# Kernel optimization log

Hardware: AMD Instinct MI355X
Metric: run time of the kernel (lower is better)

The kernel has to match this reference:

```python
import jax, jax.numpy as jnp
import numpy as np

# --- config constants (from working_memory config) ---
R = 3.9; STRENGTH = 0.1; N_ITER = 10                      # logistic map
I0 = 1.0; OMEGA = 1.0; KWAVE = 2.0; ALPHA_BASE = 1.0      # Padilha wave
LC = 0.5; DE = 2.0; CHIRP_N = 1; AMIN = 0.1; AMAX = 3.0
FD = 1.5; T = 0.0                                          # fractal dim, time
ATT_ALPHA = 1.5; EPS = 1e-10                               # spectral filter
FCI = 0.7; STAB = 0.8; DEMAND = 0.6                        # neurotransmitter drives
BASE = 0.5; SENS = 1.0; DECAY = 0.1

B, S, D4 = 4, 2048, 1024  # batch, seq_len (= memory_size), embed_dim*4


def hamilton(a, b):
    # quaternion (Hamilton) product; last dim split into 4 component blocks
    aw, ax, ay, az = jnp.split(a, 4, axis=-1)
    bw, bx, by, bz = jnp.split(b, 4, axis=-1)
    w = aw * bw - ax * bx - ay * by - az * bz
    x = aw * bx + ax * bw + ay * bz - az * by
    y = aw * by - ax * bz + ay * bw + az * bx
    z = aw * bz + ax * by - ay * bx + az * bw
    return jnp.concatenate([w, x, y, z], axis=-1)


def setup_inputs() -> dict:
    key = jax.random.key(0)
    ks = jax.random.split(key, 8)
    sc = 0.02
    return {
        "query": jax.random.normal(ks[0], (B, S, D4), jnp.float32),
        "memory": jax.random.normal(ks[1], (B, S, D4), jnp.float32),
        "Wq": jax.random.normal(ks[2], (D4, D4), jnp.float32) * sc,
        "bq": jnp.zeros((D4,), jnp.float32),
        "Wk": jax.random.normal(ks[3], (D4, D4), jnp.float32) * sc,
        "bk": jnp.zeros((D4,), jnp.float32),
        "Wv": jax.random.normal(ks[4], (D4, D4), jnp.float32) * sc,
        "bv": jnp.zeros((D4,), jnp.float32),
    }


def reference(query, memory, Wq, bq, Wk, bk, Wv, bv):
    # 1) chaotic modulation of query (logistic map on sigmoid(||x||))
    s = jax.nn.sigmoid(jnp.linalg.norm(query, axis=-1))  # [B,S]
    for _ in range(N_ITER):
        s = R * s * (1.0 - s)
    q = query * (1.0 + STRENGTH * (s[..., None] - 0.5))

    # 2) Padilha wave modulation along sequence
    seq = q.shape[1]
    alpha = float(np.clip(ALPHA_BASE * (1.0 + LC * (FD - DE) / DE), AMIN, AMAX))
    beta = 2 * CHIRP_N + 1 - 2 * FD
    lam = jnp.arange(seq, dtype=q.dtype) / seq
    wave = I0 * jnp.sin(OMEGA * T + alpha * lam) * jnp.cos(OMEGA * T - KWAVE * lam + beta * lam ** 2)
    q = q * (1.0 + 0.1 * wave[None, :, None])

    # 3) neurotransmitter scalar modulation of memory (one decay step from baseline)
    dop = (1 - DECAY) * BASE + DECAY * jax.nn.sigmoid(jnp.float32(FCI * SENS))
    ser = (1 - DECAY) * BASE + DECAY * jax.nn.sigmoid(jnp.float32(STAB * SENS))
    nor = (1 - DECAY) * BASE + DECAY * jax.nn.sigmoid(jnp.float32(DEMAND * SENS))
    mem = memory * (0.4 * dop + 0.3 * ser + 0.3 * nor)

    # 4) quaternionic spectral attention
    Q = q @ Wq.T + bq
    K = mem @ Wk.T + bk
    V = mem @ Wv.T + bv
    Qf = jnp.fft.fft(Q, axis=-2)
    Kf = jnp.fft.fft(K, axis=-2)
    Vf = jnp.fft.fft(V, axis=-2)
    kidx = jnp.arange(seq, dtype=jnp.float32)
    filt = jnp.exp(1j * ATT_ALPHA * jnp.arctan(jnp.log(kidx + EPS)))[None, :, None]
    QK = hamilton(Qf * filt, Kf * filt)
    QKV = hamilton(QK, Vf * filt)
    attended = jnp.fft.ifft(QKV, axis=-2).real.astype(query.dtype)
    return attended
```

## Files before the change

### kernel.cpp

```cpp
#include <hip/hip_runtime.h>
#include <hip/hip_fp16.h>
#include <math.h>

#define S 2048
#define D4 1024
#define NB 4
#define HS 1026
#define TWOPI 6.283185307179586f

typedef __attribute__((ext_vector_type(8))) short bf16x8;
typedef __attribute__((ext_vector_type(4))) float f32x4;

__device__ __forceinline__ float2 cmul(float2 a, float2 b){
  return make_float2(a.x*b.x - a.y*b.y, a.x*b.y + a.y*b.x);
}
__device__ __forceinline__ float2 cadd(float2 a, float2 b){ return make_float2(a.x+b.x, a.y+b.y); }
__device__ __forceinline__ float2 csub(float2 a, float2 b){ return make_float2(a.x-b.x, a.y-b.y); }

__device__ __forceinline__ unsigned short f2bf(float f){
  unsigned int u = __builtin_bit_cast(unsigned int, f);
  unsigned int r = (u + 0x7FFFu + ((u >> 16) & 1u)) >> 16;
  return (unsigned short)r;
}
__device__ __forceinline__ float bf2f(unsigned short u){
  unsigned int x = (unsigned int)u << 16;
  return __builtin_bit_cast(float, x);
}

__device__ __forceinline__ void gld16(const unsigned short* g, unsigned short* l){
  __builtin_amdgcn_global_load_lds((const __attribute__((address_space(1))) unsigned int*)g,
                                   (__attribute__((address_space(3))) unsigned int*)l,
                                   16, 0, 0);
}

__device__ __forceinline__ float2 twf(const float* twr, const float* twi, int m){
  int mm = m & 1023;
  float s = (m & 1024) ? -1.f : 1.f;
  int p = mm + (mm >> 5);
  return make_float2(s * twr[p], s * twi[p]);
}

__device__ __forceinline__ void dft8_fwd(const float2 a[8], float2 o[8]){
  const float RH = 0.70710678118654752f;
  float2 b0 = cadd(a[0],a[4]), b1 = cadd(a[1],a[5]), b2 = cadd(a[2],a[6]), b3 = cadd(a[3],a[7]);
  float2 c0 = csub(a[0],a[4]);
  float2 t1 = csub(a[1],a[5]);
  float2 c1 = make_float2(RH*(t1.x + t1.y), RH*(t1.y - t1.x));
  float2 t2 = csub(a[2],a[6]);
  float2 c2 = make_float2(t2.y, -t2.x);
  float2 t3 = csub(a[3],a[7]);
  float2 c3 = make_float2(RH*(t3.y - t3.x), RH*(-(t3.x + t3.y)));
  float2 e0 = cadd(b0,b2), e1 = cadd(b1,b3);
  float2 f0 = csub(b0,b2);
  float2 f1t = csub(b1,b3); float2 f1 = make_float2(f1t.y, -f1t.x);
  o[0] = cadd(e0,e1); o[4] = csub(e0,e1);
  o[2] = cadd(f0,f1); o[6] = csub(f0,f1);
  float2 g0 = cadd(c0,c2), g1 = cadd(c1,c3);
  float2 h0 = csub(c0,c2);
  float2 h1t = csub(c1,c3); float2 h1 = make_float2(h1t.y, -h1t.x);
  o[1] = cadd(g0,g1); o[5] = csub(g0,g1);
  o[3] = cadd(h0,h1); o[7] = csub(h0,h1);
}

__device__ __forceinline__ void dft4_fwd(const float2 a[4], float2 o[4]){
  float2 b0 = cadd(a[0],a[2]), b1 = cadd(a[1],a[3]);
  float2 c0 = csub(a[0],a[2]);
  float2 c1t = csub(a[1],a[3]); float2 c1 = make_float2(c1t.y, -c1t.x);
  o[0]=cadd(b0,b1); o[2]=csub(b0,b1); o[1]=cadd(c0,c1); o[3]=csub(c0,c1);
}
__device__ __forceinline__ void dft4_inv(const float2 a[4], float2 o[4]){
  float2 b0 = cadd(a[0],a[2]), b1 = cadd(a[1],a[3]);
  float2 c0 = csub(a[0],a[2]);
  float2 c1t = csub(a[1],a[3]); float2 c1 = make_float2(-c1t.y, c1t.x);
  o[0]=cadd(b0,b1); o[2]=csub(b0,b1); o[1]=cadd(c0,c1); o[3]=csub(c0,c1);
}

__global__ __launch_bounds__(256) void prep_kernel(float* __restrict__ scale,
                                                   float2* __restrict__ gfilt,
                                                   float2* __restrict__ twg,
                                                   float alpha, float beta){
  int i = blockIdx.x * 256 + threadIdx.x;
  float lam = (float)i / (float)S;
  float w = sinf(alpha * lam) * cosf(-2.0f * lam + beta * lam * lam);
  scale[i] = 0.95f * (1.0f + 0.1f * w);
  if (i <= 1024){
    int im = (2048 - i) & 2047;
    float th1 = 1.5f * atanf(logf((float)i  + 1e-10f));
    float th2 = 1.5f * atanf(logf((float)im + 1e-10f));
    float s1, c1, s2, c2;
    sincosf(3.0f * th1, &s1, &c1);
    sincosf(3.0f * th2, &s2, &c2);
    gfilt[i] = make_float2((c1 + c2) * 0.5f, (s1 - s2) * 0.5f);
  }
  if (i < 1024){
    float s2, c2; sincosf((float)i * (TWOPI / 2048.f), &s2, &c2);
    twg[i]        = make_float2(c2, -s2);
    twg[1024 + i] = make_float2(c2,  s2);
  }
}

__global__ __launch_bounds__(256) void convert_all(const float* __restrict__ q,
                                                   const float* __restrict__ mem,
                                                   const float* __restrict__ Wq,
                                                   const float* __restrict__ Wk,
                                                   const float* __restrict__ Wv,
                                                   unsigned short* __restrict__ XqB,
                                                   unsigned short* __restrict__ XmB,
                                                   unsigned short* __restrict__ Wall,
                                                   const float* __restrict__ scale,
                                                   float cmem){
  int bid = blockIdx.x;
  if (bid < 8192){
    size_t i = ((size_t)bid * 256 + threadIdx.x) * 4;
    int s = (int)((i / D4) % S);
    float scl = scale[s];
    float4 v = *(const float4*)&q[i];
    ushort4 o;
    o.x = f2bf(v.x * scl); o.y = f2bf(v.y * scl);
    o.z = f2bf(v.z * scl); o.w = f2bf(v.w * scl);
    *(ushort4*)&XqB[i] = o;
  } else if (bid < 16384){
    size_t i = ((size_t)(bid - 8192) * 256 + threadIdx.x) * 4;
    float4 v = *(const float4*)&mem[i];
    ushort4 o;
    o.x = f2bf(v.x * cmem); o.y = f2bf(v.y * cmem);
    o.z = f2bf(v.z * cmem); o.w = f2bf(v.w * cmem);
    *(ushort4*)&XmB[i] = o;
  } else {
    int r = bid - 16384;
    int tensor = r >> 10;
    const float* Wsrc = (tensor == 0) ? Wq : (tensor == 1 ? Wk : Wv);
    size_t i = ((size_t)(r & 1023) * 256 + threadIdx.x) * 4;
    float4 v = *(const float4*)&Wsrc[i];
    ushort4 o;
    o.x = f2bf(v.x); o.y = f2bf(v.y);
    o.z = f2bf(v.z); o.w = f2bf(v.w);
    *(ushort4*)&(Wall + (size_t)tensor * D4 * D4)[i] = o;
  }
}

#define TM 128
#define TN 128
#define TKK 64
__global__ __launch_bounds__(256) void mfma_gemm_all(const unsigned short* __restrict__ Wall,
                                                     const unsigned short* __restrict__ XqB,
                                                     const unsigned short* __restrict__ XmB,
                                                     const float* __restrict__ bq,
                                                     const float* __restrict__ bk,
                                                     const float* __restrict__ bv,
                                                     unsigned short* __restrict__ Xb){
  __shared__ unsigned short sA[2][TM * TKK];
  __shared__ unsigned short sB[2][TN * TKK];
  const int z = blockIdx.z;
  const int tensor = z >> 2, b = z & 3;
  const size_t TEN = (size_t)NB * D4 * S;
  const unsigned short* A = Wall + (size_t)tensor * D4 * D4;
  const unsigned short* B = (tensor == 0 ? XqB : XmB) + (size_t)b * S * D4;
  const float* bias = (tensor == 0) ? bq : (tensor == 1 ? bk : bv);
  unsigned short* dst = Xb + (size_t)tensor * TEN + (size_t)b * D4 * S;
  const int m0 = blockIdx.y * TM;
  const int n0 = blockIdx.x * TN;
  const int t = threadIdx.x;
  const int w = t >> 6, l = t & 63;
  const int sr = l >> 3;
  const int sc = ((l & 7) ^ sr) * 8;
  const int wr = (w >> 1) * 64;
  const int wc = (w & 1) * 64;
  const int l15 = l & 15, lh = l >> 4;
  const int co0 = ((lh     ^ (l15 & 7)) * 8);
  const int co1 = (((4+lh) ^ (l15 & 7)) * 8);

  const unsigned short* gA = A + (size_t)(m0 + w * 32 + sr) * D4 + sc;
  const unsigned short* gB = B + (size_t)(n0 + w * 32 + sr) * D4 + sc;

  f32x4 acc[4][4] = {};

#define STAGE(buf, k0) do { \
    _Pragma("unroll") \
    for (int i_ = 0; i_ < 4; ++i_){ \
      gld16(gA + (k0) + (size_t)(8 * i_) * D4, &sA[buf][w * 2048 + i_ * 512]); \
      gld16(gB + (k0) + (size_t)(8 * i_) * D4, &sB[buf][w * 2048 + i_ * 512]); \
    } \
  } while(0)

#define COMPUTE(buf) do { \
    bf16x8 bfr0[4], bfr1[4]; \
    _Pragma("unroll") \
    for (int j_ = 0; j_ < 4; ++j_){ \
      int rb = (wc + j_ * 16 + l15) * TKK; \
      bfr0[j_] = *(const bf16x8*)&sB[buf][rb + co0]; \
      bfr1[j_] = *(const bf16x8*)&sB[buf][rb + co1]; \
    } \
    _Pragma("unroll") \
    for (int i_ = 0; i_ < 4; ++i_){ \
      int ra = (wr + i_ * 16 + l15) * TKK; \
      bf16x8 af0 = *(const bf16x8*)&sA[buf][ra + co0]; \
      bf16x8 af1 = *(const bf16x8*)&sA[buf][ra + co1]; \
      _Pragma("unroll") \
      for (int j_ = 0; j_ < 4; ++j_){ \
        acc[i_][j_] = __builtin_amdgcn_mfma_f32_16x16x32_bf16(af0, bfr0[j_], acc[i_][j_], 0, 0, 0); \
        acc[i_][j_] = __builtin_amdgcn_mfma_f32_16x16x32_bf16(af1, bfr1[j_], acc[i_][j_], 0, 0, 0); \
      } \
    } \
  } while(0)

  STAGE(0, 0);
  __syncthreads();
  #pragma unroll 1
  for (int k0 = 0; k0 < 16; ++k0){
    if (k0 < 15) STAGE((k0 + 1) & 1, (k0 + 1) * TKK);
    COMPUTE(k0 & 1);
    __syncthreads();
  }

#undef STAGE
#undef COMPUTE

  #pragma unroll
  for (int i = 0; i < 4; ++i){
    int mbase = m0 + wr + i * 16 + lh * 4;
    #pragma unroll
    for (int r = 0; r < 4; ++r){
      float bi = bias[mbase + r];
      unsigned short* drow = dst + (size_t)(mbase + r) * S + n0 + wc + l15;
      #pragma unroll
      for (int j = 0; j < 4; ++j)
        drow[j * 16] = f2bf(acc[i][j][r] + bi);
    }
  }
}

__global__ __launch_bounds__(256) void fftfwd2(const unsigned short* __restrict__ src,
                                               const float2* __restrict__ twg,
                                               __half2* __restrict__ hs){
  __shared__ float zr[2112], zi[2112];
  __shared__ float twr[1056], twi[1056];
  const int t = threadIdx.x;
  #pragma unroll
  for (int q = 0; q < 4; ++q){
    int m = t + 256 * q;
    float2 wv = twg[m];
    int p = m + (m >> 5);
    twr[p] = wv.x; twi[p] = wv.y;
  }
  const unsigned short* col0 = src + (size_t)(2 * blockIdx.x) * S;
  const unsigned short* col1 = col0 + S;
  float2 v[8], o[8];
  #pragma unroll
  for (int j = 0; j < 8; ++j)
    v[j] = make_float2(bf2f(col0[t + 256 * j]), bf2f(col1[t + 256 * j]));
  dft8_fwd(v, o);
  #pragma unroll
  for (int j = 0; j < 8; ++j){ int x = 8 * t + j; zr[x + (x>>5)] = o[j].x; zi[x + (x>>5)] = o[j].y; }
  __syncthreads();
  {
    int k = t & 7;
    #pragma unroll
    for (int l = 0; l < 8; ++l){ int x = t + 256 * l; v[l] = make_float2(zr[x + (x>>5)], zi[x + (x>>5)]); }
    #pragma unroll
    for (int l = 1; l < 8; ++l) v[l] = cmul(v[l], twf(twr, twi, 32 * l * k));
    dft8_fwd(v, o);
    __syncthreads();
    int base = 8 * t - 7 * k;
    #pragma unroll
    for (int j = 0; j < 8; ++j){ int x = base + 8 * j; zr[x + (x>>5)] = o[j].x; zi[x + (x>>5)] = o[j].y; }
  }
  __syncthreads();
  {
    int k = t & 63;
    #pragma unroll
    for (int l = 0; l < 8; ++l){ int x = t + 256 * l; v[l] = make_float2(zr[x + (x>>5)], zi[x + (x>>5)]); }
    #pragma unroll
    for (int l = 1; l < 8; ++l) v[l] = cmul(v[l], twf(twr, twi, 4 * l * k));
    dft8_fwd(v, o);
    __syncthreads();
    int base = 8 * t - 7 * k;
    #pragma unroll
    for (int j = 0; j < 8; ++j){ int x = base + 64 * j; zr[x + (x>>5)] = o[j].x; zi[x + (x>>5)] = o[j].y; }
  }
  __syncthreads();
  {
    float2 a[4], oa[4], bb[4], ob[4];
    #pragma unroll
    for (int l = 0; l < 4; ++l){
      int xa = t + 512 * l;        a[l]  = make_float2(zr[xa + (xa>>5)], zi[xa + (xa>>5)]);
      int xb = t + 256 + 512 * l;  bb[l] = make_float2(zr[xb + (xb>>5)], zi[xb + (xb>>5)]);
    }
    #pragma unroll
    for (int l = 1; l < 4; ++l){
      a[l]  = cmul(a[l],  twf(twr, twi, l * t));
      bb[l] = cmul(bb[l], twf(twr, twi, l * (t + 256)));
    }
    dft4_fwd(a, oa); dft4_fwd(bb, ob);
    __syncthreads();
    #pragma unroll
    for (int j = 0; j < 4; ++j){
      int xa = t + 512 * j;        zr[xa + (xa>>5)] = oa[j].x; zi[xa + (xa>>5)] = oa[j].y;
      int xb = t + 256 + 512 * j;  zr[xb + (xb>>5)] = ob[j].x; zi[xb + (xb>>5)] = ob[j].y;
    }
  }
  __syncthreads();
  __half2* h0 = hs + (size_t)(2 * blockIdx.x) * HS;
  __half2* h1 = h0 + HS;
  #pragma unroll
  for (int q = 0; q < 4; ++q){
    int k = t + 256 * q;
    int km = (2048 - k) & 2047;
    float2 Zk = make_float2(zr[k + (k>>5)],  zi[k + (k>>5)]);
    float2 Zm = make_float2(zr[km + (km>>5)], zi[km + (km>>5)]);
    h0[k] = __float22half2_rn(make_float2(0.5f * (Zk.x + Zm.x), 0.5f * (Zk.y - Zm.y)));
    h1[k] = __float22half2_rn(make_float2(0.5f * (Zk.y + Zm.y), 0.5f * (Zm.x - Zk.x)));
  }
  if (t == 0){
    float2 Zk = make_float2(zr[1024 + (1024>>5)], zi[1024 + (1024>>5)]);
    h0[1024] = __float22half2_rn(make_float2(Zk.x, 0.f));
    h1[1024] = __float22half2_rn(make_float2(Zk.y, 0.f));
  }
}

__global__ __launch_bounds__(512) void hamifft3(const __half2* __restrict__ hs,
                                                const float2* __restrict__ gfilt,
                                                const float2* __restrict__ twg,
                                                __half* __restrict__ oreal){
  __shared__ __half2 h2s[4][1025];
  __shared__ float zr[2][1056], zi[2][1056];
  __shared__ float twr[1056], twi[1056];
  const int t = threadIdx.x;
  const int b = blockIdx.x >> 8;
  const int j = blockIdx.x & 255;
  #pragma unroll
  for (int q = 0; q < 2; ++q){
    int m = t + 512 * q;
    float2 wv = twg[m];
    int p = m + (m >> 5);
    twr[p] = wv.x; twi[p] = wv.y;
  }
  const size_t CH = (size_t)256 * HS;
  const size_t cQ = ((size_t)b * D4 + j) * HS;
  const size_t cK = cQ + (size_t)NB * D4 * HS;
  const size_t cV = cK + (size_t)NB * D4 * HS;
  const float inv2048 = 1.0f / 2048.0f;
  for (int pass = 0; pass < 3; ++pass){
    int f;
    if (pass < 2) f = t + 512 * pass;
    else { if (t != 0) break; f = 1024; }
    float2 q0 = __half22float2(hs[cQ + f]),        q1 = __half22float2(hs[cQ + CH + f]),
           q2 = __half22float2(hs[cQ + 2*CH + f]), q3 = __half22float2(hs[cQ + 3*CH + f]);
    float2 k0 = __half22float2(hs[cK + f]),        k1 = __half22float2(hs[cK + CH + f]),
           k2 = __half22float2(hs[cK + 2*CH + f]), k3 = __half22float2(hs[cK + 3*CH + f]);
    float2 v0 = __half22float2(hs[cV + f]),        v1 = __half22float2(hs[cV + CH + f]),
           v2 = __half22float2(hs[cV + 2*CH + f]), v3 = __half22float2(hs[cV + 3*CH + f]);
    float2 hw = csub(csub(csub(cmul(q0,k0), cmul(q1,k1)), cmul(q2,k2)), cmul(q3,k3));
    float2 hx = csub(cadd(cadd(cmul(q0,k1), cmul(q1,k0)), cmul(q2,k3)), cmul(q3,k2));
    float2 hy = cadd(cadd(csub(cmul(q0,k2), cmul(q1,k3)), cmul(q2,k0)), cmul(q3,k1));
    float2 hz = csub(cadd(cadd(cmul(q0,k3), cmul(q1,k2)), cmul(q3,k0)), cmul(q2,k1));
    float2 ow = csub(csub(csub(cmul(hw,v0), cmul(hx,v1)), cmul(hy,v2)), cmul(hz,v3));
    float2 ox = csub(cadd(cadd(cmul(hw,v1), cmul(hx,v0)), cmul(hy,v3)), cmul(hz,v2));
    float2 oy = cadd(cadd(csub(cmul(hw,v2), cmul(hx,v3)), cmul(hy,v0)), cmul(hz,v1));
    float2 oz = csub(cadd(cadd(cmul(hw,v3), cmul(hx,v2)), cmul(hz,v0)), cmul(hy,v1));
    h2s[0][f] = __float22half2_rn(make_float2(ow.x * inv2048, ow.y * inv2048));
    h2s[1][f] = __float22half2_rn(make_float2(ox.x * inv2048, ox.y * inv2048));
    h2s[2][f] = __float22half2_rn(make_float2(oy.x * inv2048, oy.y * inv2048));
    h2s[3][f] = __float22half2_rn(make_float2(oz.x * inv2048, oz.y * inv2048));
  }
  __syncthreads();

  const int h = t >> 8;
  const int tt = t & 255;
  float* hzr = zr[h]; float* hzi = zi[h];
  for (int cc = 0; cc < 2; ++cc){
    const int c = 2 * cc + h;
    #pragma unroll
    for (int q = 0; q < 4; ++q){
      int k = tt + 256 * q;
      float2 ya = cmul(__half22float2(h2s[c][k]),        gfilt[k]);
      float2 yb = cmul(__half22float2(h2s[c][1024 - k]), gfilt[1024 - k]);
      float2 ybc = make_float2(yb.x, -yb.y);
      float2 e = cadd(ya, ybc);
      float2 od = csub(ya, ybc);
      float2 wv = twf(twr, twi, k);
      float2 wo = cmul(wv, od);
      zr[h][k + (k>>5)] = e.x - wo.y;
      zi[h][k + (k>>5)] = e.y + wo.x;
    }
    __syncthreads();
    #pragma unroll
    for (int s = 0; s < 5; ++s){
      const int p = 1 << (2 * s);
      float2 a[4], o4[4];
      #pragma unroll
      for (int l = 0; l < 4; ++l){ int x = tt + 256 * l; a[l] = make_float2(hzr[x + (x>>5)], hzi[x + (x>>5)]); }
      int k = tt & (p - 1);
      int mstep = k * (512 / p);
      #pragma unroll
      for (int l = 1; l < 4; ++l) a[l] = cmul(a[l], twf(twr, twi, l * mstep));
      dft4_inv(a, o4);
      __syncthreads();
      int base = 4 * tt - 3 * k;
      #pragma unroll
      for (int j2 = 0; j2 < 4; ++j2){ int x = base + j2 * p; hzr[x + (x>>5)] = o4[j2].x; hzi[x + (x>>5)] = o4[j2].y; }
      __syncthreads();
    }
    __half2* ocol2 = (__half2*)(oreal + ((size_t)b * D4 + (j + 256 * c)) * S);
    #pragma unroll
    for (int q = 0; q < 4; ++q){
      int n = tt + 256 * q;
      ocol2[n] = __float22half2_rn(make_float2(hzr[n + (n>>5)], hzi[n + (n>>5)]));
    }
    __syncthreads();
  }
}

__global__ __launch_bounds__(256) void transpose_kernel(const __half* __restrict__ src,
                                                        float* __restrict__ out){
  __shared__ float tile[32][33];
  const int b  = blockIdx.z;
  const int s0 = blockIdx.x * 32;
  const int d0 = blockIdx.y * 32;
  const int tx = threadIdx.x, ty = threadIdx.y;
  #pragma unroll
  for (int i = 0; i < 32; i += 8)
    tile[ty + i][tx] = __half2float(src[((size_t)(b * D4 + d0 + ty + i)) * S + (s0 + tx)]);
  __syncthreads();
  #pragma unroll
  for (int i = 0; i < 32; i += 8)
    out[((size_t)(b * S + s0 + ty + i)) * D4 + (d0 + tx)] = tile[tx][ty + i];
}

extern "C" void kernel_launch(void* const* d_in, const int* in_sizes, int n_in,
                              void* d_out, int out_size, void* d_ws, size_t ws_size,
                              hipStream_t stream){
  const float* query  = (const float*)d_in[0];
  const float* memory = (const float*)d_in[1];
  const float* Wq = (const float*)d_in[2];
  const float* bq = (const float*)d_in[3];
  const float* Wk = (const float*)d_in[4];
  const float* bk = (const float*)d_in[5];
  const float* Wv = (const float*)d_in[6];
  const float* bv = (const float*)d_in[7];
  float* out = (float*)d_out;

  const size_t TEN = (size_t)NB * D4 * S;
  unsigned short* Xb = (unsigned short*)d_ws;
  __half* oreal = (__half*)(Xb + 3 * TEN);
  float* wsScale = (float*)(oreal + TEN);
  float2* wsGfilt = (float2*)(wsScale + S);
  float2* wsTwg   = wsGfilt + S;
  char* A0 = (char*)(wsTwg + S);
  unsigned short* XqB  = (unsigned short*)A0;
  unsigned short* XmB  = XqB + TEN;
  unsigned short* Wall = XmB + TEN;
  __half2* hs = (__half2*)A0;

  double dop = 0.45 + 0.1 / (1.0 + exp(-0.7));
  double ser = 0.45 + 0.1 / (1.0 + exp(-0.8));
  double nor = 0.45 + 0.1 / (1.0 + exp(-0.6));
  float cmem = (float)(0.4 * dop + 0.3 * ser + 0.3 * nor);
  float alpha = 0.875f, beta = 0.0f;

  prep_kernel<<<8, 256, 0, stream>>>(wsScale, wsGfilt, wsTwg, alpha, beta);

  convert_all<<<19456, 256, 0, stream>>>(query, memory, Wq, Wk, Wv,
                                         XqB, XmB, Wall, wsScale, cmem);

  dim3 gg(S / TN, D4 / TM, 12);
  mfma_gemm_all<<<gg, 256, 0, stream>>>(Wall, XqB, XmB, bq, bk, bv, Xb);

  fftfwd2<<<3 * NB * D4 / 2, 256, 0, stream>>>(Xb, wsTwg, hs);

  hamifft3<<<NB * 256, 512, 0, stream>>>(hs, wsGfilt, wsTwg + 1024, oreal);

  dim3 tg(S / 32, D4 / 32, NB);
  transpose_kernel<<<tg, dim3(32, 8), 0, stream>>>(oreal, out);
}
```

Measured before the change: 157.4 us.

## Enlarge GEMM tile to 128x256 with 8 waves and triple-buffered LDS pipeline

The bf16 MFMA projection GEMM now uses a 128x256 output tile with 512 threads (8 waves in a 2x4 grid) and a three-stage LDS ring. Two tiles are prefetched ahead, with explicit vmcnt waits plus barriers replacing __syncthreads. s_setprio is raised around the MFMA block. The aim is to hide global load latency and get more reuse per loaded A tile, at the cost of more LDS per block (about 144 KB) and therefore lower occupancy.

```diff
diff --git a/kernel.cpp b/kernel.cpp
--- a/kernel.cpp
+++ b/kernel.cpp
@@ -140,17 +140,17 @@
 }
 
 #define TM 128
-#define TN 128
+#define TN 256
 #define TKK 64
-__global__ __launch_bounds__(256) void mfma_gemm_all(const unsigned short* __restrict__ Wall,
+__global__ __launch_bounds__(512) void mfma_gemm_all(const unsigned short* __restrict__ Wall,
                                                      const unsigned short* __restrict__ XqB,
                                                      const unsigned short* __restrict__ XmB,
                                                      const float* __restrict__ bq,
                                                      const float* __restrict__ bk,
                                                      const float* __restrict__ bv,
                                                      unsigned short* __restrict__ Xb){
-  __shared__ unsigned short sA[2][TM * TKK];
-  __shared__ unsigned short sB[2][TN * TKK];
+  __shared__ unsigned short sA[3 * TM * TKK];
+  __shared__ unsigned short sB[3 * TN * TKK];
   const int z = blockIdx.z;
   const int tensor = z >> 2, b = z & 3;
   const size_t TEN = (size_t)NB * D4 * S;
@@ -162,55 +162,62 @@
   const int n0 = blockIdx.x * TN;
   const int t = threadIdx.x;
   const int w = t >> 6, l = t & 63;
-  const int sr = l >> 3;
-  const int sc = ((l & 7) ^ sr) * 8;
-  const int wr = (w >> 1) * 64;
-  const int wc = (w & 1) * 64;
+  const int wm = w >> 2, wn = w & 3;
+  const int tr = t >> 3;
+  const int sc = ((t & 7) ^ (tr & 7)) * 8;
+  const int ldst = tr * TKK + (t & 7) * 8;
   const int l15 = l & 15, lh = l >> 4;
   const int co0 = ((lh     ^ (l15 & 7)) * 8);
   const int co1 = (((4+lh) ^ (l15 & 7)) * 8);
 
-  const unsigned short* gA = A + (size_t)(m0 + w * 32 + sr) * D4 + sc;
-  const unsigned short* gB = B + (size_t)(n0 + w * 32 + sr) * D4 + sc;
-
   f32x4 acc[4][4] = {};
 
-#define STAGE(buf, k0) do { \
+#define STAGE(bi, k0) do { \
     _Pragma("unroll") \
-    for (int i_ = 0; i_ < 4; ++i_){ \
-      gld16(gA + (k0) + (size_t)(8 * i_) * D4, &sA[buf][w * 2048 + i_ * 512]); \
-      gld16(gB + (k0) + (size_t)(8 * i_) * D4, &sB[buf][w * 2048 + i_ * 512]); \
-    } \
+    for (int r_ = 0; r_ < 2; ++r_) \
+      gld16(A + (size_t)(m0 + r_ * 64 + tr) * D4 + (k0) + sc, \
+            &sA[(bi) * (TM * TKK) + r_ * 64 * TKK + ldst]); \
+    _Pragma("unroll") \
+    for (int r_ = 0; r_ < 4; ++r_) \
+      gld16(B + (size_t)(n0 + r_ * 64 + tr) * D4 + (k0) + sc, \
+            &sB[(bi) * (TN * TKK) + r_ * 64 * TKK + ldst]); \
   } while(0)
 
-#define COMPUTE(buf) do { \
+#define COMPUTE(bi) do { \
+    const unsigned short* bA = &sA[(bi) * (TM * TKK)]; \
+    const unsigned short* bB = &sB[(bi) * (TN * TKK)]; \
     bf16x8 bfr0[4], bfr1[4]; \
     _Pragma("unroll") \
     for (int j_ = 0; j_ < 4; ++j_){ \
-      int rb = (wc + j_ * 16 + l15) * TKK; \
-      bfr0[j_] = *(const bf16x8*)&sB[buf][rb + co0]; \
-      bfr1[j_] = *(const bf16x8*)&sB[buf][rb + co1]; \
+      int rb = (wn * 64 + j_ * 16 + l15) * TKK; \
+      bfr0[j_] = *(const bf16x8*)&bB[rb + co0]; \
+      bfr1[j_] = *(const bf16x8*)&bB[rb + co1]; \
     } \
+    __builtin_amdgcn_s_setprio(1); \
     _Pragma("unroll") \
     for (int i_ = 0; i_ < 4; ++i_){ \
-      int ra = (wr + i_ * 16 + l15) * TKK; \
-      bf16x8 af0 = *(const bf16x8*)&sA[buf][ra + co0]; \
-      bf16x8 af1 = *(const bf16x8*)&sA[buf][ra + co1]; \
+      int ra = (wm * 64 + i_ * 16 + l15) * TKK; \
+      bf16x8 af0 = *(const bf16x8*)&bA[ra + co0]; \
+      bf16x8 af1 = *(const bf16x8*)&bA[ra + co1]; \
       _Pragma("unroll") \
       for (int j_ = 0; j_ < 4; ++j_){ \
         acc[i_][j_] = __builtin_amdgcn_mfma_f32_16x16x32_bf16(af0, bfr0[j_], acc[i_][j_], 0, 0, 0); \
         acc[i_][j_] = __builtin_amdgcn_mfma_f32_16x16x32_bf16(af1, bfr1[j_], acc[i_][j_], 0, 0, 0); \
       } \
     } \
+    __builtin_amdgcn_s_setprio(0); \
   } while(0)
 
   STAGE(0, 0);
-  __syncthreads();
+  STAGE(1, TKK);
+  asm volatile("s_waitcnt vmcnt(6)\n\ts_barrier" ::: "memory");
+
   #pragma unroll 1
-  for (int k0 = 0; k0 < 16; ++k0){
-    if (k0 < 15) STAGE((k0 + 1) & 1, (k0 + 1) * TKK);
-    COMPUTE(k0 & 1);
-    __syncthreads();
+  for (int kt = 0; kt < 16; ++kt){
+    if (kt < 14) STAGE((kt + 2) % 3, (kt + 2) * TKK);
+    COMPUTE(kt % 3);
+    if (kt < 14)      asm volatile("s_waitcnt vmcnt(6)\n\ts_barrier" ::: "memory");
+    else if (kt == 14) asm volatile("s_waitcnt vmcnt(0)\n\ts_barrier" ::: "memory");
   }
 
 #undef STAGE
@@ -218,11 +225,11 @@
 
   #pragma unroll
   for (int i = 0; i < 4; ++i){
-    int mbase = m0 + wr + i * 16 + lh * 4;
+    int mbase = m0 + wm * 64 + i * 16 + lh * 4;
     #pragma unroll
     for (int r = 0; r < 4; ++r){
       float bi = bias[mbase + r];
-      unsigned short* drow = dst + (size_t)(mbase + r) * S + n0 + wc + l15;
+      unsigned short* drow = dst + (size_t)(mbase + r) * S + n0 + wn * 64 + l15;
       #pragma unroll
       for (int j = 0; j < 4; ++j)
         drow[j * 16] = f2bf(acc[i][j][r] + bi);
@@ -464,7 +471,7 @@
                                          XqB, XmB, Wall, wsScale, cmem);
 
   dim3 gg(S / TN, D4 / TM, 12);
-  mfma_gemm_all<<<gg, 256, 0, stream>>>(Wall, XqB, XmB, bq, bk, bv, Xb);
+  mfma_gemm_all<<<gg, 512, 0, stream>>>(Wall, XqB, XmB, bq, bk, bv, Xb);
 
   fftfwd2<<<3 * NB * D4 / 2, 256, 0, stream>>>(Xb, wsTwg, hs);
 
```

Result: slower. 169.3 us (+7.6%).
